# Kernel optimization log

Hardware: AMD Instinct MI355X
Metric: run time of the kernel (lower is better)

The kernel has to match this reference:

```python
import jax, jax.numpy as jnp
import numpy as np

B, S, D, K, ITERS = 16, 4096, 1024, 16, 3
SCALE = D ** -0.5
EPS_LN = 1e-5
EPS_ATTN = 1e-8


def setup_inputs() -> dict:
    key = jax.random.key(0)
    ks = jax.random.split(key, 16)

    def lin_w(k, out_d, in_d):
        return (jax.random.uniform(k, (out_d, in_d)) * 2 - 1) / np.sqrt(in_d)

    return {
        "tokens": jax.random.normal(ks[0], (B, S, D), dtype=jnp.float32),
        "slot_mu": jax.random.normal(ks[1], (1, K, D), dtype=jnp.float32) * 0.02,
        "Wq": lin_w(ks[2], D, D), "bq": jnp.zeros((D,), jnp.float32),
        "Wk": lin_w(ks[3], D, D), "bk": jnp.zeros((D,), jnp.float32),
        "Wv": lin_w(ks[4], D, D), "bv": jnp.zeros((D,), jnp.float32),
        "W_ih": lin_w(ks[5], 3 * D, D), "b_ih": jnp.zeros((3 * D,), jnp.float32),
        "W_hh": lin_w(ks[6], 3 * D, D), "b_hh": jnp.zeros((3 * D,), jnp.float32),
        "W1": lin_w(ks[7], 4 * D, D), "b1": jnp.zeros((4 * D,), jnp.float32),
        "W2": lin_w(ks[8], D, 4 * D), "b2": jnp.zeros((D,), jnp.float32),
        "g_slots": jnp.ones((D,), jnp.float32), "b_slots": jnp.zeros((D,), jnp.float32),
        "g_mlp": jnp.ones((D,), jnp.float32), "b_mlp": jnp.zeros((D,), jnp.float32),
    }


def _ln(x, g, b):
    mu = jnp.mean(x, axis=-1, keepdims=True)
    var = jnp.mean(jnp.square(x - mu), axis=-1, keepdims=True)
    return (x - mu) * jax.lax.rsqrt(var + EPS_LN) * g + b


def reference(tokens, slot_mu, Wq, bq, Wk, bk, Wv, bv,
              W_ih, b_ih, W_hh, b_hh, W1, b1, W2, b2,
              g_slots, b_slots, g_mlp, b_mlp):
    # eval-mode slot init: slots = mu (no reparameterization noise)
    slots = jnp.broadcast_to(slot_mu, (tokens.shape[0], K, D))
    k = tokens @ Wk.T + bk  # (B,S,D)
    v = tokens @ Wv.T + bv  # (B,S,D)
    attn = None
    for _ in range(ITERS):
        slots_prev = slots
        q = _ln(slots, g_slots, b_slots) @ Wq.T + bq            # (B,K,D)
        logits = jnp.einsum('bkd,bsd->bks', q, k) * SCALE        # (B,K,S)
        attn = jax.nn.softmax(logits, axis=1)                    # softmax over slots K
        attn_n = attn / (jnp.sum(attn, axis=2, keepdims=True) + EPS_ATTN)
        updates = jnp.einsum('bks,bsd->bkd', attn_n, v)          # (B,K,D)
        # GRUCell(updates, slots_prev)
        gi = updates @ W_ih.T + b_ih                             # (B,K,3D)
        gh = slots_prev @ W_hh.T + b_hh
        ir, iz, in_ = jnp.split(gi, 3, axis=-1)
        hr, hz, hn = jnp.split(gh, 3, axis=-1)
        r = jax.nn.sigmoid(ir + hr)
        z = jax.nn.sigmoid(iz + hz)
        n = jnp.tanh(in_ + r * hn)
        slots = (1.0 - z) * n + z * slots_prev
        # MLP residual
        h = _ln(slots, g_mlp, b_mlp)
        slots = slots + jax.nn.gelu(h @ W1.T + b1, approximate=False) @ W2.T + b2
    return slots, attn
```

## Files before the change

kernel.cpp:

```cpp
#include <hip/hip_runtime.h>


typedef unsigned short u16;
typedef unsigned int u32;
typedef float f32x4 __attribute__((ext_vector_type(4)));
typedef unsigned int u32x2 __attribute__((ext_vector_type(2)));
typedef unsigned int u32x4 __attribute__((ext_vector_type(4)));
typedef __bf16 bf16x8 __attribute__((ext_vector_type(8)));

#define B_ 16
#define S_ 4096
#define D_ 1024
#define K_ 16
#define SCALE_ 0.03125f

__device__ __forceinline__ float b2f(u16 u) {
  u32 x = ((u32)u) << 16;
  return __builtin_bit_cast(float, x);
}
__device__ __forceinline__ u16 f2b(float f) {
  u32 u = __builtin_bit_cast(u32, f);
  u32 r = (u + 0x7fffu + ((u >> 16) & 1u)) >> 16;
  return (u16)r;
}
__device__ __forceinline__ bf16x8 ld16g(const u16* p) {
  return __builtin_bit_cast(bf16x8, *(const u32x4*)p);
}
__device__ __forceinline__ void gload_lds16(const void* g, void* l) {
  __builtin_amdgcn_global_load_lds(
      (const __attribute__((address_space(1))) void*)g,
      (__attribute__((address_space(3))) void*)l, 16, 0, 0);
}

__global__ void convert8_kernel(const float* __restrict__ src,
                                u16* __restrict__ dst, int n8) {
  const int idx = blockIdx.x * 256 + threadIdx.x;
  if (idx >= n8) return;
  const float* s = src + (size_t)idx * 8;
  const f32x4 lo = *(const f32x4*)s;
  const f32x4 hi = *(const f32x4*)(s + 4);
  union { u16 h[8]; u32x4 q; } u;
#pragma unroll
  for (int j = 0; j < 4; ++j) { u.h[j] = f2b(lo[j]); u.h[4 + j] = f2b(hi[j]); }
  *(u32x4*)(dst + (size_t)idx * 8) = u.q;
}

__global__ __launch_bounds__(256) void transcvt_kernel(
    const float* __restrict__ src, u16* __restrict__ dst, int R, int C) {
  const int r0 = blockIdx.x * 64;
  const int c0 = blockIdx.y * 64;
  const int cl = threadIdx.x & 63;
  const int rq = threadIdx.x >> 6;
#pragma unroll
  for (int h = 0; h < 2; ++h) {
    const int rbase = (rq + h * 4) * 8;
    union { u16 u[8]; u32x4 q; } w;
#pragma unroll
    for (int j = 0; j < 8; ++j)
      w.u[j] = f2b(src[(size_t)(r0 + rbase + j) * C + c0 + cl]);
    *(u32x4*)&dst[(size_t)(c0 + cl) * R + r0 + rbase] = w.q;
  }
}

__global__ void colvec_kernel(const float* __restrict__ W,
                              const float* __restrict__ x,
                              float* __restrict__ out, int R, int C) {
  const int c = blockIdx.x * 256 + threadIdx.x;
  const int r0 = blockIdx.y * 64;
  if (c >= C) return;
  float acc = 0.f;
#pragma unroll 8
  for (int r = 0; r < 64; ++r)
    acc = fmaf(W[(size_t)(r0 + r) * C + c], x[r0 + r], acc);
  atomicAdd(&out[c], acc);
}

__global__ __launch_bounds__(256) void rowvec_kernel(
    const float* __restrict__ W, const float* __restrict__ x,
    const float* __restrict__ add, float* __restrict__ out, int R, int C) {
  const int wave = threadIdx.x >> 6, lane = threadIdx.x & 63;
  const int r = blockIdx.x * 4 + wave;
  if (r >= R) return;
  float acc = 0.f;
  for (int c = lane; c < C; c += 64) acc = fmaf(W[(size_t)r * C + c], x[c], acc);
#pragma unroll
  for (int off = 1; off < 64; off <<= 1) acc += __shfl_xor(acc, off);
  if (lane == 0) out[r] = add[r] + acc;
}

__global__ __launch_bounds__(256) void gemm128_bb(
    const u16* __restrict__ A, const u16* __restrict__ Bw,
    const float* __restrict__ bias, u16* __restrict__ C, int N, int Kd,
    int mtiles) {
  __shared__ __align__(16) u16 At[128 * 64];
  __shared__ __align__(16) u16 Bt[128 * 64];
  const int tid = threadIdx.x;
  const int ntiles = N >> 7;
  const int nwg = mtiles * ntiles;
  const int cpx = nwg >> 3;
  const int lin = blockIdx.x;
  const int wg = (lin & 7) * cpx + (lin >> 3);
  const int m0 = (wg / ntiles) * 128;
  const int n0 = (wg % ntiles) * 128;
  const int wave = tid >> 6, lane = tid & 63;
  const int q4 = lane >> 4, l16 = lane & 15;
  const int wm = (wave & 1) * 64, wn = (wave >> 1) * 64;

  f32x4 acc[4][4];
#pragma unroll
  for (int i = 0; i < 4; ++i)
#pragma unroll
    for (int j = 0; j < 4; ++j) acc[i][j] = 0.f;

  const int trow = tid >> 3;
  const int tcol = ((tid & 7) * 8) ^ ((trow & 7) << 3);
  const u16* ga = A + (size_t)(m0 + trow) * Kd + tcol;
  const u16* gb = Bw + (size_t)(n0 + trow) * Kd + tcol;
  u16* la = At + tid * 8;
  u16* lb = Bt + tid * 8;

  for (int k0 = 0; k0 < Kd; k0 += 64) {
    __syncthreads();
#pragma unroll
    for (int c = 0; c < 4; ++c)
      gload_lds16(ga + (size_t)c * 32 * Kd + k0, la + c * 2048);
#pragma unroll
    for (int c = 0; c < 4; ++c)
      gload_lds16(gb + (size_t)c * 32 * Kd + k0, lb + c * 2048);
    __syncthreads();
#pragma unroll
    for (int kk = 0; kk < 64; kk += 32) {
      bf16x8 af[4], bfr[4];
#pragma unroll
      for (int i = 0; i < 4; ++i) {
        const int row = wm + i * 16 + l16;
        const int byo = row * 128 + ((kk * 2 + q4 * 16) ^ ((row & 7) << 4));
        af[i] = *(const bf16x8*)((const char*)At + byo);
      }
#pragma unroll
      for (int j = 0; j < 4; ++j) {
        const int row = wn + j * 16 + l16;
        const int byo = row * 128 + ((kk * 2 + q4 * 16) ^ ((row & 7) << 4));
        bfr[j] = *(const bf16x8*)((const char*)Bt + byo);
      }
#pragma unroll
      for (int i = 0; i < 4; ++i)
#pragma unroll
        for (int j = 0; j < 4; ++j)
          acc[i][j] = __builtin_amdgcn_mfma_f32_16x16x32_bf16(af[i], bfr[j],
                                                              acc[i][j], 0, 0, 0);
    }
  }
#pragma unroll
  for (int j = 0; j < 4; ++j) {
    const int col = n0 + wn + j * 16 + l16;
    const float bv = bias ? bias[col] : 0.f;
#pragma unroll
    for (int i = 0; i < 4; ++i) {
      const int rowb = m0 + wm + i * 16 + q4 * 4;
#pragma unroll
      for (int r = 0; r < 4; ++r)
        C[(size_t)(rowb + r) * N + col] = f2b(acc[i][j][r] + bv);
    }
  }
}

template <int MODE>
__global__ __launch_bounds__(256) void gemm64_bt(
    const u16* __restrict__ A, const u16* __restrict__ Bw,
    const float* __restrict__ bias, float* Cf, u16* Cb, const float* resid,
    int N, int Kd) {
  __shared__ __align__(16) u16 At[64 * 64];
  __shared__ __align__(16) u16 Bt[64 * 64];
  const int tid = threadIdx.x;
  const int m0 = blockIdx.x * 64;
  const int n0 = blockIdx.y * 64;
  const int wave = tid >> 6, lane = tid & 63;
  const int q4 = lane >> 4, l16 = lane & 15;
  const int wm = (wave & 1) * 32, wn = (wave >> 1) * 32;

  f32x4 acc[2][2];
#pragma unroll
  for (int i = 0; i < 2; ++i)
#pragma unroll
    for (int j = 0; j < 2; ++j) acc[i][j] = 0.f;

  const int r_ = tid >> 3;
  const int c8 = (tid & 7) * 8;
  const int c8s = c8 ^ ((r_ & 7) << 3);

  for (int k0 = 0; k0 < Kd; k0 += 64) {
    u32x4 ta[2], tb[2];
#pragma unroll
    for (int i = 0; i < 2; ++i) {
      ta[i] = *(const u32x4*)(A + (size_t)(m0 + r_ + i * 32) * Kd + k0 + c8);
      tb[i] = *(const u32x4*)(Bw + (size_t)(n0 + r_ + i * 32) * Kd + k0 + c8);
    }
    __syncthreads();
#pragma unroll
    for (int i = 0; i < 2; ++i) {
      *(u32x4*)&At[(r_ + i * 32) * 64 + c8s] = ta[i];
      *(u32x4*)&Bt[(r_ + i * 32) * 64 + c8s] = tb[i];
    }
    __syncthreads();
#pragma unroll
    for (int kk = 0; kk < 64; kk += 32) {
      bf16x8 af[2], bfr[2];
#pragma unroll
      for (int i = 0; i < 2; ++i) {
        const int row = wm + i * 16 + l16;
        const int byo = row * 128 + ((kk * 2 + q4 * 16) ^ ((row & 7) << 4));
        af[i] = *(const bf16x8*)((const char*)At + byo);
      }
#pragma unroll
      for (int j = 0; j < 2; ++j) {
        const int row = wn + j * 16 + l16;
        const int byo = row * 128 + ((kk * 2 + q4 * 16) ^ ((row & 7) << 4));
        bfr[j] = *(const bf16x8*)((const char*)Bt + byo);
      }
#pragma unroll
      for (int i = 0; i < 2; ++i)
#pragma unroll
        for (int j = 0; j < 2; ++j)
          acc[i][j] = __builtin_amdgcn_mfma_f32_16x16x32_bf16(af[i], bfr[j],
                                                              acc[i][j], 0, 0, 0);
    }
  }
#pragma unroll
  for (int j = 0; j < 2; ++j) {
    const int col = n0 + wn + j * 16 + l16;
    const float bv = bias[col];
#pragma unroll
    for (int i = 0; i < 2; ++i) {
      const int rowb = m0 + wm + i * 16 + q4 * 4;
#pragma unroll
      for (int r = 0; r < 4; ++r) {
        const int row = rowb + r;
        float val = acc[i][j][r] + bv;
        if constexpr (MODE == 0) {
          Cb[(size_t)row * N + col] = f2b(val);
        } else if constexpr (MODE == 2) {
          val = 0.5f * val * (1.f + erff(val * 0.70710678118654752f));
          Cb[(size_t)row * N + col] = f2b(val);
        } else {
          const float rv = resid[(size_t)row * N + col];
          Cf[(size_t)row * N + col] = val + rv;
        }
      }
    }
  }
}

__global__ __launch_bounds__(256) void gemm64_dual(
    const u16* __restrict__ A0, const u16* __restrict__ A1,
    const u16* __restrict__ B0, const u16* __restrict__ B1,
    const float* __restrict__ bias0, const float* __restrict__ bias1,
    float* C0, float* C1, int N, int Kd) {
  const u16* A = blockIdx.z ? A1 : A0;
  const u16* Bw = blockIdx.z ? B1 : B0;
  const float* bias = blockIdx.z ? bias1 : bias0;
  float* Cf = blockIdx.z ? C1 : C0;
  __shared__ __align__(16) u16 At[64 * 64];
  __shared__ __align__(16) u16 Bt[64 * 64];
  const int tid = threadIdx.x;
  const int m0 = blockIdx.x * 64;
  const int n0 = blockIdx.y * 64;
  const int wave = tid >> 6, lane = tid & 63;
  const int q4 = lane >> 4, l16 = lane & 15;
  const int wm = (wave & 1) * 32, wn = (wave >> 1) * 32;

  f32x4 acc[2][2];
#pragma unroll
  for (int i = 0; i < 2; ++i)
#pragma unroll
    for (int j = 0; j < 2; ++j) acc[i][j] = 0.f;

  const int r_ = tid >> 3;
  const int c8 = (tid & 7) * 8;
  const int c8s = c8 ^ ((r_ & 7) << 3);

  for (int k0 = 0; k0 < Kd; k0 += 64) {
    u32x4 ta[2], tb[2];
#pragma unroll
    for (int i = 0; i < 2; ++i) {
      ta[i] = *(const u32x4*)(A + (size_t)(m0 + r_ + i * 32) * Kd + k0 + c8);
      tb[i] = *(const u32x4*)(Bw + (size_t)(n0 + r_ + i * 32) * Kd + k0 + c8);
    }
    __syncthreads();
#pragma unroll
    for (int i = 0; i < 2; ++i) {
      *(u32x4*)&At[(r_ + i * 32) * 64 + c8s] = ta[i];
      *(u32x4*)&Bt[(r_ + i * 32) * 64 + c8s] = tb[i];
    }
    __syncthreads();
#pragma unroll
    for (int kk = 0; kk < 64; kk += 32) {
      bf16x8 af[2], bfr[2];
#pragma unroll
      for (int i = 0; i < 2; ++i) {
        const int row = wm + i * 16 + l16;
        const int byo = row * 128 + ((kk * 2 + q4 * 16) ^ ((row & 7) << 4));
        af[i] = *(const bf16x8*)((const char*)At + byo);
      }
#pragma unroll
      for (int j = 0; j < 2; ++j) {
        const int row = wn + j * 16 + l16;
        const int byo = row * 128 + ((kk * 2 + q4 * 16) ^ ((row & 7) << 4));
        bfr[j] = *(const bf16x8*)((const char*)Bt + byo);
      }
#pragma unroll
      for (int i = 0; i < 2; ++i)
#pragma unroll
        for (int j = 0; j < 2; ++j)
          acc[i][j] = __builtin_amdgcn_mfma_f32_16x16x32_bf16(af[i], bfr[j],
                                                              acc[i][j], 0, 0, 0);
    }
  }
#pragma unroll
  for (int j = 0; j < 2; ++j) {
    const int col = n0 + wn + j * 16 + l16;
    const float bv = bias[col];
#pragma unroll
    for (int i = 0; i < 2; ++i) {
      const int rowb = m0 + wm + i * 16 + q4 * 4;
#pragma unroll
      for (int r = 0; r < 4; ++r)
        Cf[(size_t)(rowb + r) * N + col] = acc[i][j][r] + bv;
    }
  }
}

__global__ __launch_bounds__(256) void attn_fused(
    const u16* __restrict__ qb, const u16* __restrict__ tok,
    const float* __restrict__ qdot, float* __restrict__ rowsum,
    float* __restrict__ updates, float* __restrict__ attn_out) {
  __shared__ float p_lds[256][20];
  const int b = blockIdx.y;
  const int wave = threadIdx.x >> 6, lane = threadIdx.x & 63;
  const int q4 = lane >> 4, l16 = lane & 15;
  const int tokbase = blockIdx.x * 256;
  const int tok0 = tokbase + wave * 64;
  const u16* ap = qb + (size_t)(b * 16 + l16) * D_ + q4 * 8;
  const u16* bp = tok + ((size_t)b * S_ + tok0 + l16) * D_ + q4 * 8;
  const f32x4 qd = *(const f32x4*)&qdot[b * 16 + q4 * 4];
  f32x4 acc[4];
#pragma unroll
  for (int j = 0; j < 4; ++j) acc[j] = 0.f;
  for (int k0 = 0; k0 < D_; k0 += 32) {
    bf16x8 a = ld16g(ap + k0);
#pragma unroll
    for (int j = 0; j < 4; ++j) {
      bf16x8 bb = ld16g(bp + (size_t)j * 16 * D_ + k0);
      acc[j] = __builtin_amdgcn_mfma_f32_16x16x32_bf16(a, bb, acc[j], 0, 0, 0);
    }
  }
  float rs[4] = {0.f, 0.f, 0.f, 0.f};
#pragma unroll
  for (int j = 0; j < 4; ++j) {
    const int tl = wave * 64 + j * 16 + l16;
    float l[4];
#pragma unroll
    for (int r = 0; r < 4; ++r) l[r] = (acc[j][r] + qd[r]) * SCALE_;
    float mx = fmaxf(fmaxf(l[0], l[1]), fmaxf(l[2], l[3]));
    mx = fmaxf(mx, __shfl_xor(mx, 16));
    mx = fmaxf(mx, __shfl_xor(mx, 32));
    float e[4], ssum = 0.f;
#pragma unroll
    for (int r = 0; r < 4; ++r) { e[r] = __expf(l[r] - mx); ssum += e[r]; }
    ssum += __shfl_xor(ssum, 16);
    ssum += __shfl_xor(ssum, 32);
    const float inv = 1.f / ssum;
    f32x4 p;
#pragma unroll
    for (int r = 0; r < 4; ++r) { p[r] = e[r] * inv; rs[r] += p[r]; }
    *(f32x4*)&p_lds[tl][q4 * 4] = p;
    if (attn_out) {
#pragma unroll
      for (int r = 0; r < 4; ++r)
        attn_out[(size_t)(b * 16 + q4 * 4 + r) * S_ + tokbase + tl] = p[r];
    }
  }
#pragma unroll
  for (int r = 0; r < 4; ++r) {
    float v = rs[r];
    v += __shfl_xor(v, 1);
    v += __shfl_xor(v, 2);
    v += __shfl_xor(v, 4);
    v += __shfl_xor(v, 8);
    if (l16 == 0) atomicAdd(&rowsum[b * 16 + q4 * 4 + r], v);
  }
  __syncthreads();
  const int d = threadIdx.x * 4;
  const u16* tp = tok + ((size_t)b * S_ + tokbase) * D_ + d;
  f32x4 acc2[16];
#pragma unroll
  for (int k = 0; k < 16; ++k) acc2[k] = 0.f;
#pragma unroll 2
  for (int s = 0; s < 256; ++s) {
    const u32x2 w = *(const u32x2*)(tp + (size_t)s * D_);
    const float v0 = b2f((u16)(w[0] & 0xffffu));
    const float v1 = b2f((u16)(w[0] >> 16));
    const float v2 = b2f((u16)(w[1] & 0xffffu));
    const float v3 = b2f((u16)(w[1] >> 16));
#pragma unroll
    for (int k4 = 0; k4 < 4; ++k4) {
      const f32x4 pv = *(const f32x4*)&p_lds[s][k4 * 4];
#pragma unroll
      for (int r = 0; r < 4; ++r) {
        const int k = k4 * 4 + r;
        acc2[k][0] = fmaf(pv[r], v0, acc2[k][0]);
        acc2[k][1] = fmaf(pv[r], v1, acc2[k][1]);
        acc2[k][2] = fmaf(pv[r], v2, acc2[k][2]);
        acc2[k][3] = fmaf(pv[r], v3, acc2[k][3]);
      }
    }
  }
  float* up = updates + (size_t)(b * 16) * D_ + d;
#pragma unroll
  for (int k = 0; k < 16; ++k) {
#pragma unroll
    for (int c = 0; c < 4; ++c)
      atomicAdd(&up[(size_t)k * D_ + c], acc2[k][c]);
  }
}

__global__ void normcvt_kernel(float* __restrict__ updates,
                               const float* __restrict__ rowsum,
                               u16* __restrict__ out) {
  const int idx = blockIdx.x * 256 + threadIdx.x;
  const int m = idx >> 10;
  const float inv = 1.f / (rowsum[m] + 1e-8f);
  out[idx] = f2b(updates[idx] * inv);
  updates[idx] = 0.f;
}

__global__ __launch_bounds__(256) void ln_kernel(
    const float* __restrict__ x, const float* __restrict__ g,
    const float* __restrict__ bb, u16* __restrict__ out_ln,
    u16* __restrict__ out_raw, const float* __restrict__ qd_w,
    float* __restrict__ qdot_out, float* __restrict__ rowsum_zero) {
  const int row = blockIdx.x, tid = threadIdx.x;
  const float* xr = x + (size_t)row * D_;
  float v[4], s = 0.f, ss = 0.f;
#pragma unroll
  for (int i = 0; i < 4; ++i) {
    v[i] = xr[tid + i * 256];
    s += v[i];
    ss += v[i] * v[i];
  }
#pragma unroll
  for (int off = 1; off < 64; off <<= 1) {
    s += __shfl_xor(s, off);
    ss += __shfl_xor(ss, off);
  }
  __shared__ float sh[8];
  __shared__ float shq[4];
  if ((tid & 63) == 0) { sh[tid >> 6] = s; sh[4 + (tid >> 6)] = ss; }
  __syncthreads();
  s = sh[0] + sh[1] + sh[2] + sh[3];
  ss = sh[4] + sh[5] + sh[6] + sh[7];
  const float mu = s * (1.f / 1024.f);
  float var = ss * (1.f / 1024.f) - mu * mu;
  var = fmaxf(var, 0.f);
  const float rstd = rsqrtf(var + 1e-5f);
  float qa = 0.f;
#pragma unroll
  for (int i = 0; i < 4; ++i) {
    const int dd = tid + i * 256;
    const float lv = (v[i] - mu) * rstd * g[dd] + bb[dd];
    out_ln[(size_t)row * D_ + dd] = f2b(lv);
    if (out_raw) out_raw[(size_t)row * D_ + dd] = f2b(v[i]);
    if (qd_w) qa = fmaf(lv, qd_w[dd], qa);
  }
  if (qd_w) {
#pragma unroll
    for (int off = 1; off < 64; off <<= 1) qa += __shfl_xor(qa, off);
    if ((tid & 63) == 0) shq[tid >> 6] = qa;
    __syncthreads();
    if (tid == 0) qdot_out[row] = shq[0] + shq[1] + shq[2] + shq[3];
  }
  if (rowsum_zero && tid == 0) rowsum_zero[row] = 0.f;
}

__global__ __launch_bounds__(256) void gru_ln_kernel(
    const float* __restrict__ gi, const float* __restrict__ gh,
    float* __restrict__ slots, const float* __restrict__ g,
    const float* __restrict__ bb, u16* __restrict__ out_ln) {
  const int row = blockIdx.x, tid = threadIdx.x;
  const size_t gbase = (size_t)row * 3072;
  const size_t sbase = (size_t)row * 1024;
  float v[4], s = 0.f, ss = 0.f;
#pragma unroll
  for (int i = 0; i < 4; ++i) {
    const int dd = tid + i * 256;
    const float ir = gi[gbase + dd], iz = gi[gbase + dd + 1024],
                in_ = gi[gbase + dd + 2048];
    const float hr = gh[gbase + dd], hz = gh[gbase + dd + 1024],
                hn = gh[gbase + dd + 2048];
    const float r = 1.f / (1.f + __expf(-(ir + hr)));
    const float z = 1.f / (1.f + __expf(-(iz + hz)));
    const float n = tanhf(in_ + r * hn);
    const float sv = (1.f - z) * n + z * slots[sbase + dd];
    slots[sbase + dd] = sv;
    v[i] = sv;
    s += sv;
    ss += sv * sv;
  }
#pragma unroll
  for (int off = 1; off < 64; off <<= 1) {
    s += __shfl_xor(s, off);
    ss += __shfl_xor(ss, off);
  }
  __shared__ float sh[8];
  if ((tid & 63) == 0) { sh[tid >> 6] = s; sh[4 + (tid >> 6)] = ss; }
  __syncthreads();
  s = sh[0] + sh[1] + sh[2] + sh[3];
  ss = sh[4] + sh[5] + sh[6] + sh[7];
  const float mu = s * (1.f / 1024.f);
  float var = ss * (1.f / 1024.f) - mu * mu;
  var = fmaxf(var, 0.f);
  const float rstd = rsqrtf(var + 1e-5f);
#pragma unroll
  for (int i = 0; i < 4; ++i) {
    const int dd = tid + i * 256;
    out_ln[sbase + dd] = f2b((v[i] - mu) * rstd * g[dd] + bb[dd]);
  }
}

__global__ void init_slots_kernel(const float* __restrict__ mu,
                                  float* __restrict__ slots) {
  const int idx = blockIdx.x * 256 + threadIdx.x;
  slots[idx] = mu[idx & (K_ * D_ - 1)];
}

extern "C" void kernel_launch(void* const* d_in, const int* in_sizes, int n_in,
                              void* d_out, int out_size, void* d_ws,
                              size_t ws_size, hipStream_t stream) {
  const float* tokens = (const float*)d_in[0];
  const float* slot_mu = (const float*)d_in[1];
  const float* Wq = (const float*)d_in[2];
  const float* bq = (const float*)d_in[3];
  const float* Wk = (const float*)d_in[4];
  const float* bk = (const float*)d_in[5];
  const float* Wv = (const float*)d_in[6];
  const float* bv = (const float*)d_in[7];
  const float* W_ih = (const float*)d_in[8];
  const float* b_ih = (const float*)d_in[9];
  const float* W_hh = (const float*)d_in[10];
  const float* b_hh = (const float*)d_in[11];
  const float* W1 = (const float*)d_in[12];
  const float* b1 = (const float*)d_in[13];
  const float* W2 = (const float*)d_in[14];
  const float* b2 = (const float*)d_in[15];
  const float* g_slots = (const float*)d_in[16];
  const float* b_slots = (const float*)d_in[17];
  const float* g_mlp = (const float*)d_in[18];
  const float* b_mlp = (const float*)d_in[19];

  char* p = (char*)d_ws;
  auto alloc = [&](size_t bytes) {
    char* r = p;
    p += (bytes + 255) & ~(size_t)255;
    return r;
  };
  u16* tokb = (u16*)alloc((size_t)B_ * S_ * D_ * 2);
  float* slots = (float*)alloc((size_t)B_ * K_ * D_ * 4);
  float* updates = (float*)alloc((size_t)B_ * K_ * D_ * 4);
  float* rowsum = (float*)alloc(1024);
  float* gi = (float*)alloc((size_t)B_ * K_ * 3 * D_ * 4);
  float* gh = (float*)alloc((size_t)B_ * K_ * 3 * D_ * 4);
  u16* slots_bf16 = (u16*)alloc((size_t)B_ * K_ * D_ * 2);
  u16* slots_ln_bf16 = (u16*)alloc((size_t)B_ * K_ * D_ * 2);
  u16* qkbuf = (u16*)alloc((size_t)B_ * K_ * D_ * 2);
  u16* updates_bf16 = (u16*)alloc((size_t)B_ * K_ * D_ * 2);
  u16* h_bf16 = (u16*)alloc((size_t)B_ * K_ * D_ * 2);
  u16* act_bf16 = (u16*)alloc((size_t)B_ * K_ * 4 * D_ * 2);
  float* qdotbuf = (float*)alloc(256 * 4);
  float* qd_w = (float*)alloc(D_ * 4);
  float* qkbias = (float*)alloc(D_ * 4);
  float* bihv = (float*)alloc(3 * D_ * 4);
  u16* cWih = (u16*)alloc((size_t)3 * D_ * D_ * 2);
  u16* cWhh = (u16*)alloc((size_t)3 * D_ * D_ * 2);
  u16* cW1 = (u16*)alloc((size_t)4 * D_ * D_ * 2);
  u16* cW2 = (u16*)alloc((size_t)4 * D_ * D_ * 2);
  u16* cWqT = (u16*)alloc((size_t)D_ * D_ * 2);
  u16* cWkT = (u16*)alloc((size_t)D_ * D_ * 2);
  u16* cWvT = (u16*)alloc((size_t)D_ * D_ * 2);
  u16* cPT = (u16*)alloc((size_t)D_ * D_ * 2);
  u16* cWihv = (u16*)alloc((size_t)3 * D_ * D_ * 2);
  if ((size_t)(p - (char*)d_ws) > ws_size) return;

  float* out_slots = (float*)d_out;
  float* out_attn = (float*)d_out + (size_t)B_ * K_ * D_;

  convert8_kernel<<<(3 * D_ * D_ / 8 + 255) / 256, 256, 0, stream>>>(W_ih, cWih, 3 * D_ * D_ / 8);
  convert8_kernel<<<(3 * D_ * D_ / 8 + 255) / 256, 256, 0, stream>>>(W_hh, cWhh, 3 * D_ * D_ / 8);
  convert8_kernel<<<(4 * D_ * D_ / 8 + 255) / 256, 256, 0, stream>>>(W1, cW1, 4 * D_ * D_ / 8);
  convert8_kernel<<<(4 * D_ * D_ / 8 + 255) / 256, 256, 0, stream>>>(W2, cW2, 4 * D_ * D_ / 8);
  convert8_kernel<<<(B_ * S_ * D_ / 8 + 255) / 256, 256, 0, stream>>>(
      tokens, tokb, B_ * S_ * D_ / 8);
  transcvt_kernel<<<dim3(16, 16), 256, 0, stream>>>(Wq, cWqT, D_, D_);
  transcvt_kernel<<<dim3(16, 16), 256, 0, stream>>>(Wk, cWkT, D_, D_);
  transcvt_kernel<<<dim3(16, 16), 256, 0, stream>>>(Wv, cWvT, D_, D_);

  gemm128_bb<<<64, 256, 0, stream>>>(cWkT, cWqT, nullptr, cPT, D_, D_, 8);
  gemm128_bb<<<192, 256, 0, stream>>>(cWih, cWvT, nullptr, cWihv, D_, D_, 24);

  hipMemsetAsync(qkbias, 0, D_ * 4, stream);
  hipMemsetAsync(qd_w, 0, D_ * 4, stream);
  colvec_kernel<<<dim3(4, 16), 256, 0, stream>>>(Wk, bq, qkbias, D_, D_);
  colvec_kernel<<<dim3(4, 16), 256, 0, stream>>>(Wq, bk, qd_w, D_, D_);
  rowvec_kernel<<<768, 256, 0, stream>>>(W_ih, bv, b_ih, bihv, 3 * D_, D_);

  hipMemsetAsync(updates, 0, (size_t)B_ * K_ * D_ * 4 + 1024, stream);
  init_slots_kernel<<<1024, 256, 0, stream>>>(slot_mu, slots);

  for (int it = 0; it < 3; ++it) {
    ln_kernel<<<256, 256, 0, stream>>>(slots, g_slots, b_slots, slots_ln_bf16,
                                       slots_bf16, qd_w, qdotbuf, rowsum);
    gemm64_bt<0><<<dim3(4, 16), 256, 0, stream>>>(slots_ln_bf16, cPT, qkbias,
                                                  nullptr, qkbuf, nullptr, D_, D_);
    attn_fused<<<dim3(16, 16), 256, 0, stream>>>(
        qkbuf, tokb, qdotbuf, rowsum, updates, (it == 2) ? out_attn : nullptr);
    normcvt_kernel<<<1024, 256, 0, stream>>>(updates, rowsum, updates_bf16);
    gemm64_dual<<<dim3(4, 48, 2), 256, 0, stream>>>(
        updates_bf16, slots_bf16, cWihv, cWhh, bihv, b_hh, gi, gh, 3 * D_, D_);
    gru_ln_kernel<<<256, 256, 0, stream>>>(gi, gh, slots, g_mlp, b_mlp, h_bf16);
    gemm64_bt<2><<<dim3(4, 64), 256, 0, stream>>>(h_bf16, cW1, b1, nullptr,
                                                  act_bf16, nullptr, 4 * D_, D_);
    gemm64_bt<3><<<dim3(4, 16), 256, 0, stream>>>(
        act_bf16, cW2, b2, (it == 2) ? out_slots : slots, nullptr, slots, D_,
        4 * D_);
  }
}
```

Baseline: 1.220 ms.

## Merge setup conversion kernels, deepen GEMM K-tiles, halve attention token tile

Several independent changes are bundled. The one-time weight and token bf16 conversions, the three transposes, the two colvec products and the two precompute GEMMs are each merged into a single launch to cut launch overhead. The 64-row GEMMs now stage 128-wide K tiles per barrier instead of 64, so there are fewer sync rounds but LDS use doubles. The attention kernel processes 128 tokens per block instead of 256 and launches twice as many blocks, which adds parallelism at the cost of more atomic traffic on the updates buffer.

```diff
diff --git a/kernel.cpp b/kernel.cpp
--- a/kernel.cpp
+++ b/kernel.cpp
@@ -32,21 +32,36 @@
       (__attribute__((address_space(3))) void*)l, 16, 0, 0);
 }
 
-__global__ void convert8_kernel(const float* __restrict__ src,
-                                u16* __restrict__ dst, int n8) {
+__device__ __forceinline__ void cvt8(const float* s, u16* d, int k) {
+  const float* sp = s + (size_t)k * 8;
+  const f32x4 lo = *(const f32x4*)sp;
+  const f32x4 hi = *(const f32x4*)(sp + 4);
+  union { u16 h[8]; u32x4 q; } u;
+#pragma unroll
+  for (int j = 0; j < 4; ++j) { u.h[j] = f2b(lo[j]); u.h[4 + j] = f2b(hi[j]); }
+  *(u32x4*)(d + (size_t)k * 8) = u.q;
+}
+
+__global__ void convert_multi(const float* sA, u16* dA, int eA,
+                              const float* sB, u16* dB, int eB,
+                              const float* sC, u16* dC, int eC,
+                              const float* sD, u16* dD, int eD,
+                              const float* sE, u16* dE, int eE) {
   const int idx = blockIdx.x * 256 + threadIdx.x;
-  if (idx >= n8) return;
-  const float* s = src + (size_t)idx * 8;
-  const f32x4 lo = *(const f32x4*)s;
-  const f32x4 hi = *(const f32x4*)(s + 4);
-  union { u16 h[8]; u32x4 q; } u;
-#pragma unroll
-  for (int j = 0; j < 4; ++j) { u.h[j] = f2b(lo[j]); u.h[4 + j] = f2b(hi[j]); }
-  *(u32x4*)(dst + (size_t)idx * 8) = u.q;
-}
-
-__global__ __launch_bounds__(256) void transcvt_kernel(
-    const float* __restrict__ src, u16* __restrict__ dst, int R, int C) {
+  if (idx < eA) { cvt8(sA, dA, idx); return; }
+  if (idx < eB) { cvt8(sB, dB, idx - eA); return; }
+  if (idx < eC) { cvt8(sC, dC, idx - eB); return; }
+  if (idx < eD) { cvt8(sD, dD, idx - eC); return; }
+  if (idx < eE) { cvt8(sE, dE, idx - eD); return; }
+}
+
+__global__ __launch_bounds__(256) void transcvt3_kernel(
+    const float* __restrict__ s0, u16* __restrict__ d0,
+    const float* __restrict__ s1, u16* __restrict__ d1,
+    const float* __restrict__ s2, u16* __restrict__ d2) {
+  const float* src = blockIdx.z == 0 ? s0 : (blockIdx.z == 1 ? s1 : s2);
+  u16* dst = blockIdx.z == 0 ? d0 : (blockIdx.z == 1 ? d1 : d2);
+  const int R = D_, C = D_;
   const int r0 = blockIdx.x * 64;
   const int c0 = blockIdx.y * 64;
   const int cl = threadIdx.x & 63;
@@ -62,16 +77,21 @@
   }
 }
 
-__global__ void colvec_kernel(const float* __restrict__ W,
-                              const float* __restrict__ x,
-                              float* __restrict__ out, int R, int C) {
+__global__ void colvec2_kernel(const float* __restrict__ W0,
+                               const float* __restrict__ x0,
+                               float* __restrict__ o0,
+                               const float* __restrict__ W1,
+                               const float* __restrict__ x1,
+                               float* __restrict__ o1) {
+  const float* W = blockIdx.z ? W1 : W0;
+  const float* x = blockIdx.z ? x1 : x0;
+  float* out = blockIdx.z ? o1 : o0;
   const int c = blockIdx.x * 256 + threadIdx.x;
   const int r0 = blockIdx.y * 64;
-  if (c >= C) return;
   float acc = 0.f;
 #pragma unroll 8
   for (int r = 0; r < 64; ++r)
-    acc = fmaf(W[(size_t)(r0 + r) * C + c], x[r0 + r], acc);
+    acc = fmaf(W[(size_t)(r0 + r) * D_ + c], x[r0 + r], acc);
   atomicAdd(&out[c], acc);
 }
 
@@ -88,17 +108,13 @@
   if (lane == 0) out[r] = add[r] + acc;
 }
 
-__global__ __launch_bounds__(256) void gemm128_bb(
+__device__ __forceinline__ void gemm128_body(
     const u16* __restrict__ A, const u16* __restrict__ Bw,
-    const float* __restrict__ bias, u16* __restrict__ C, int N, int Kd,
-    int mtiles) {
-  __shared__ __align__(16) u16 At[128 * 64];
-  __shared__ __align__(16) u16 Bt[128 * 64];
+    u16* __restrict__ C, int N, int Kd, int mtiles, int lin, u16* At, u16* Bt) {
   const int tid = threadIdx.x;
   const int ntiles = N >> 7;
   const int nwg = mtiles * ntiles;
   const int cpx = nwg >> 3;
-  const int lin = blockIdx.x;
   const int wg = (lin & 7) * cpx + (lin >> 3);
   const int m0 = (wg / ntiles) * 128;
   const int n0 = (wg % ntiles) * 128;
@@ -154,15 +170,25 @@
 #pragma unroll
   for (int j = 0; j < 4; ++j) {
     const int col = n0 + wn + j * 16 + l16;
-    const float bv = bias ? bias[col] : 0.f;
 #pragma unroll
     for (int i = 0; i < 4; ++i) {
       const int rowb = m0 + wm + i * 16 + q4 * 4;
 #pragma unroll
       for (int r = 0; r < 4; ++r)
-        C[(size_t)(rowb + r) * N + col] = f2b(acc[i][j][r] + bv);
-    }
-  }
+        C[(size_t)(rowb + r) * N + col] = f2b(acc[i][j][r]);
+    }
+  }
+}
+
+__global__ __launch_bounds__(256) void gemm128_pair(
+    const u16* A0, const u16* B0, u16* C0, int mt0, int nb0,
+    const u16* A1, const u16* B1, u16* C1, int mt1) {
+  __shared__ __align__(16) u16 At[128 * 64];
+  __shared__ __align__(16) u16 Bt[128 * 64];
+  if ((int)blockIdx.x < nb0)
+    gemm128_body(A0, B0, C0, D_, D_, mt0, blockIdx.x, At, Bt);
+  else
+    gemm128_body(A1, B1, C1, D_, D_, mt1, blockIdx.x - nb0, At, Bt);
 }
 
 template <int MODE>
@@ -170,8 +196,8 @@
     const u16* __restrict__ A, const u16* __restrict__ Bw,
     const float* __restrict__ bias, float* Cf, u16* Cb, const float* resid,
     int N, int Kd) {
-  __shared__ __align__(16) u16 At[64 * 64];
-  __shared__ __align__(16) u16 Bt[64 * 64];
+  __shared__ __align__(16) u16 At[64 * 128];
+  __shared__ __align__(16) u16 Bt[64 * 128];
   const int tid = threadIdx.x;
   const int m0 = blockIdx.x * 64;
   const int n0 = blockIdx.y * 64;
@@ -185,37 +211,37 @@
 #pragma unroll
     for (int j = 0; j < 2; ++j) acc[i][j] = 0.f;
 
-  const int r_ = tid >> 3;
-  const int c8 = (tid & 7) * 8;
-  const int c8s = c8 ^ ((r_ & 7) << 3);
-
-  for (int k0 = 0; k0 < Kd; k0 += 64) {
-    u32x4 ta[2], tb[2];
-#pragma unroll
-    for (int i = 0; i < 2; ++i) {
-      ta[i] = *(const u32x4*)(A + (size_t)(m0 + r_ + i * 32) * Kd + k0 + c8);
-      tb[i] = *(const u32x4*)(Bw + (size_t)(n0 + r_ + i * 32) * Kd + k0 + c8);
+  const int r_ = tid >> 4;
+  const int c16 = (tid & 15) * 8;
+  const int c16s = c16 ^ ((r_ & 7) << 3);
+
+  for (int k0 = 0; k0 < Kd; k0 += 128) {
+    u32x4 ta[4], tb[4];
+#pragma unroll
+    for (int c = 0; c < 4; ++c) {
+      ta[c] = *(const u32x4*)(A + (size_t)(m0 + c * 16 + r_) * Kd + k0 + c16);
+      tb[c] = *(const u32x4*)(Bw + (size_t)(n0 + c * 16 + r_) * Kd + k0 + c16);
     }
     __syncthreads();
 #pragma unroll
-    for (int i = 0; i < 2; ++i) {
-      *(u32x4*)&At[(r_ + i * 32) * 64 + c8s] = ta[i];
-      *(u32x4*)&Bt[(r_ + i * 32) * 64 + c8s] = tb[i];
+    for (int c = 0; c < 4; ++c) {
+      *(u32x4*)&At[(c * 16 + r_) * 128 + c16s] = ta[c];
+      *(u32x4*)&Bt[(c * 16 + r_) * 128 + c16s] = tb[c];
     }
     __syncthreads();
 #pragma unroll
-    for (int kk = 0; kk < 64; kk += 32) {
+    for (int kk = 0; kk < 128; kk += 32) {
       bf16x8 af[2], bfr[2];
 #pragma unroll
       for (int i = 0; i < 2; ++i) {
         const int row = wm + i * 16 + l16;
-        const int byo = row * 128 + ((kk * 2 + q4 * 16) ^ ((row & 7) << 4));
+        const int byo = row * 256 + ((kk * 2 + q4 * 16) ^ ((row & 7) << 4));
         af[i] = *(const bf16x8*)((const char*)At + byo);
       }
 #pragma unroll
       for (int j = 0; j < 2; ++j) {
         const int row = wn + j * 16 + l16;
-        const int byo = row * 128 + ((kk * 2 + q4 * 16) ^ ((row & 7) << 4));
+        const int byo = row * 256 + ((kk * 2 + q4 * 16) ^ ((row & 7) << 4));
         bfr[j] = *(const bf16x8*)((const char*)Bt + byo);
       }
 #pragma unroll
@@ -260,8 +286,8 @@
   const u16* Bw = blockIdx.z ? B1 : B0;
   const float* bias = blockIdx.z ? bias1 : bias0;
   float* Cf = blockIdx.z ? C1 : C0;
-  __shared__ __align__(16) u16 At[64 * 64];
-  __shared__ __align__(16) u16 Bt[64 * 64];
+  __shared__ __align__(16) u16 At[64 * 128];
+  __shared__ __align__(16) u16 Bt[64 * 128];
   const int tid = threadIdx.x;
   const int m0 = blockIdx.x * 64;
   const int n0 = blockIdx.y * 64;
@@ -275,37 +301,37 @@
 #pragma unroll
     for (int j = 0; j < 2; ++j) acc[i][j] = 0.f;
 
-  const int r_ = tid >> 3;
-  const int c8 = (tid & 7) * 8;
-  const int c8s = c8 ^ ((r_ & 7) << 3);
-
-  for (int k0 = 0; k0 < Kd; k0 += 64) {
-    u32x4 ta[2], tb[2];
-#pragma unroll
-    for (int i = 0; i < 2; ++i) {
-      ta[i] = *(const u32x4*)(A + (size_t)(m0 + r_ + i * 32) * Kd + k0 + c8);
-      tb[i] = *(const u32x4*)(Bw + (size_t)(n0 + r_ + i * 32) * Kd + k0 + c8);
+  const int r_ = tid >> 4;
+  const int c16 = (tid & 15) * 8;
+  const int c16s = c16 ^ ((r_ & 7) << 3);
+
+  for (int k0 = 0; k0 < Kd; k0 += 128) {
+    u32x4 ta[4], tb[4];
+#pragma unroll
+    for (int c = 0; c < 4; ++c) {
+      ta[c] = *(const u32x4*)(A + (size_t)(m0 + c * 16 + r_) * Kd + k0 + c16);
+      tb[c] = *(const u32x4*)(Bw + (size_t)(n0 + c * 16 + r_) * Kd + k0 + c16);
     }
     __syncthreads();
 #pragma unroll
-    for (int i = 0; i < 2; ++i) {
-      *(u32x4*)&At[(r_ + i * 32) * 64 + c8s] = ta[i];
-      *(u32x4*)&Bt[(r_ + i * 32) * 64 + c8s] = tb[i];
+    for (int c = 0; c < 4; ++c) {
+      *(u32x4*)&At[(c * 16 + r_) * 128 + c16s] = ta[c];
+      *(u32x4*)&Bt[(c * 16 + r_) * 128 + c16s] = tb[c];
     }
     __syncthreads();
 #pragma unroll
-    for (int kk = 0; kk < 64; kk += 32) {
+    for (int kk = 0; kk < 128; kk += 32) {
       bf16x8 af[2], bfr[2];
 #pragma unroll
       for (int i = 0; i < 2; ++i) {
         const int row = wm + i * 16 + l16;
-        const int byo = row * 128 + ((kk * 2 + q4 * 16) ^ ((row & 7) << 4));
+        const int byo = row * 256 + ((kk * 2 + q4 * 16) ^ ((row & 7) << 4));
         af[i] = *(const bf16x8*)((const char*)At + byo);
       }
 #pragma unroll
       for (int j = 0; j < 2; ++j) {
         const int row = wn + j * 16 + l16;
-        const int byo = row * 128 + ((kk * 2 + q4 * 16) ^ ((row & 7) << 4));
+        const int byo = row * 256 + ((kk * 2 + q4 * 16) ^ ((row & 7) << 4));
         bfr[j] = *(const bf16x8*)((const char*)Bt + byo);
       }
 #pragma unroll
@@ -334,30 +360,30 @@
     const u16* __restrict__ qb, const u16* __restrict__ tok,
     const float* __restrict__ qdot, float* __restrict__ rowsum,
     float* __restrict__ updates, float* __restrict__ attn_out) {
-  __shared__ float p_lds[256][20];
+  __shared__ float p_lds[128][20];
   const int b = blockIdx.y;
   const int wave = threadIdx.x >> 6, lane = threadIdx.x & 63;
   const int q4 = lane >> 4, l16 = lane & 15;
-  const int tokbase = blockIdx.x * 256;
-  const int tok0 = tokbase + wave * 64;
+  const int tokbase = blockIdx.x * 128;
+  const int tok0 = tokbase + wave * 32;
   const u16* ap = qb + (size_t)(b * 16 + l16) * D_ + q4 * 8;
   const u16* bp = tok + ((size_t)b * S_ + tok0 + l16) * D_ + q4 * 8;
   const f32x4 qd = *(const f32x4*)&qdot[b * 16 + q4 * 4];
-  f32x4 acc[4];
-#pragma unroll
-  for (int j = 0; j < 4; ++j) acc[j] = 0.f;
+  f32x4 acc[2];
+#pragma unroll
+  for (int j = 0; j < 2; ++j) acc[j] = 0.f;
   for (int k0 = 0; k0 < D_; k0 += 32) {
     bf16x8 a = ld16g(ap + k0);
 #pragma unroll
-    for (int j = 0; j < 4; ++j) {
+    for (int j = 0; j < 2; ++j) {
       bf16x8 bb = ld16g(bp + (size_t)j * 16 * D_ + k0);
       acc[j] = __builtin_amdgcn_mfma_f32_16x16x32_bf16(a, bb, acc[j], 0, 0, 0);
     }
   }
   float rs[4] = {0.f, 0.f, 0.f, 0.f};
 #pragma unroll
-  for (int j = 0; j < 4; ++j) {
-    const int tl = wave * 64 + j * 16 + l16;
+  for (int j = 0; j < 2; ++j) {
+    const int tl = wave * 32 + j * 16 + l16;
     float l[4];
 #pragma unroll
     for (int r = 0; r < 4; ++r) l[r] = (acc[j][r] + qd[r]) * SCALE_;
@@ -396,7 +422,7 @@
 #pragma unroll
   for (int k = 0; k < 16; ++k) acc2[k] = 0.f;
 #pragma unroll 2
-  for (int s = 0; s < 256; ++s) {
+  for (int s = 0; s < 128; ++s) {
     const u32x2 w = *(const u32x2*)(tp + (size_t)s * D_);
     const float v0 = b2f((u16)(w[0] & 0xffffu));
     const float v1 = b2f((u16)(w[0] >> 16));
@@ -593,23 +619,21 @@
   float* out_slots = (float*)d_out;
   float* out_attn = (float*)d_out + (size_t)B_ * K_ * D_;
 
-  convert8_kernel<<<(3 * D_ * D_ / 8 + 255) / 256, 256, 0, stream>>>(W_ih, cWih, 3 * D_ * D_ / 8);
-  convert8_kernel<<<(3 * D_ * D_ / 8 + 255) / 256, 256, 0, stream>>>(W_hh, cWhh, 3 * D_ * D_ / 8);
-  convert8_kernel<<<(4 * D_ * D_ / 8 + 255) / 256, 256, 0, stream>>>(W1, cW1, 4 * D_ * D_ / 8);
-  convert8_kernel<<<(4 * D_ * D_ / 8 + 255) / 256, 256, 0, stream>>>(W2, cW2, 4 * D_ * D_ / 8);
-  convert8_kernel<<<(B_ * S_ * D_ / 8 + 255) / 256, 256, 0, stream>>>(
-      tokens, tokb, B_ * S_ * D_ / 8);
-  transcvt_kernel<<<dim3(16, 16), 256, 0, stream>>>(Wq, cWqT, D_, D_);
-  transcvt_kernel<<<dim3(16, 16), 256, 0, stream>>>(Wk, cWkT, D_, D_);
-  transcvt_kernel<<<dim3(16, 16), 256, 0, stream>>>(Wv, cWvT, D_, D_);
-
-  gemm128_bb<<<64, 256, 0, stream>>>(cWkT, cWqT, nullptr, cPT, D_, D_, 8);
-  gemm128_bb<<<192, 256, 0, stream>>>(cWih, cWvT, nullptr, cWihv, D_, D_, 24);
-
+  const int eA = 3 * D_ * D_ / 8;
+  const int eB = eA + 3 * D_ * D_ / 8;
+  const int eC = eB + 4 * D_ * D_ / 8;
+  const int eD = eC + 4 * D_ * D_ / 8;
+  const int eE = eD + B_ * S_ * D_ / 8;
+  convert_multi<<<(eE + 255) / 256, 256, 0, stream>>>(
+      W_ih, cWih, eA, W_hh, cWhh, eB, W1, cW1, eC, W2, cW2, eD, tokens, tokb, eE);
+  transcvt3_kernel<<<dim3(16, 16, 3), 256, 0, stream>>>(Wq, cWqT, Wk, cWkT,
+                                                        Wv, cWvT);
+  gemm128_pair<<<256, 256, 0, stream>>>(cWkT, cWqT, cPT, 8, 64,
+                                        cWih, cWvT, cWihv, 24);
   hipMemsetAsync(qkbias, 0, D_ * 4, stream);
   hipMemsetAsync(qd_w, 0, D_ * 4, stream);
-  colvec_kernel<<<dim3(4, 16), 256, 0, stream>>>(Wk, bq, qkbias, D_, D_);
-  colvec_kernel<<<dim3(4, 16), 256, 0, stream>>>(Wq, bk, qd_w, D_, D_);
+  colvec2_kernel<<<dim3(4, 16, 2), 256, 0, stream>>>(Wk, bq, qkbias,
+                                                     Wq, bk, qd_w);
   rowvec_kernel<<<768, 256, 0, stream>>>(W_ih, bv, b_ih, bihv, 3 * D_, D_);
 
   hipMemsetAsync(updates, 0, (size_t)B_ * K_ * D_ * 4 + 1024, stream);
@@ -620,7 +644,7 @@
                                        slots_bf16, qd_w, qdotbuf, rowsum);
     gemm64_bt<0><<<dim3(4, 16), 256, 0, stream>>>(slots_ln_bf16, cPT, qkbias,
                                                   nullptr, qkbuf, nullptr, D_, D_);
-    attn_fused<<<dim3(16, 16), 256, 0, stream>>>(
+    attn_fused<<<dim3(32, 16), 256, 0, stream>>>(
         qkbuf, tokb, qdotbuf, rowsum, updates, (it == 2) ? out_attn : nullptr);
     normcvt_kernel<<<1024, 256, 0, stream>>>(updates, rowsum, updates_bf16);
     gemm64_dual<<<dim3(4, 48, 2), 256, 0, stream>>>(
```

Result: no change. 1.244 ms (+2.0%).
